# Optimization experiments

Measured on AMD Instinct MI355X. Metric: run time of the kernel, lower is better.

Reference implementation:

```python
import jax, jax.numpy as jnp
import numpy as np
import math

H_IMG, W_IMG = 800, 1216
STRIDES = [4, 8, 16, 32, 64]
SIZES = [32, 64, 128, 256, 512]
RATIOS = [0.5, 1.0, 2.0]
NUM_PER_LEVEL = [(-(-H_IMG // s)) * (-(-W_IMG // s)) * len(RATIOS) for s in STRIDES]
A_TOTAL = sum(NUM_PER_LEVEL)  # 728973
B = 4
PRE_NMS = 1000   # pre_nms_top_n['testing']
POST_NMS = 1000  # post_nms_top_n['testing']
NMS_TH = 0.7
MIN_SIZE = 1e-3
BBOX_XFORM_CLIP = math.log(1000.0 / 16)
NEG = -1e10
LEVELS_NP = np.repeat(np.arange(len(NUM_PER_LEVEL)), NUM_PER_LEVEL).astype(np.int32)


def _make_anchors():
    out = []
    for stride, size in zip(STRIDES, SIZES):
        fh, fw = -(-H_IMG // stride), -(-W_IMG // stride)
        r = np.sqrt(np.asarray(RATIOS, dtype=np.float64))
        ws, hs = size / r, size * r
        base = np.stack([-ws / 2, -hs / 2, ws / 2, hs / 2], axis=1)  # [3,4]
        sx = np.arange(fw, dtype=np.float64) * stride
        sy = np.arange(fh, dtype=np.float64) * stride
        gy, gx = np.meshgrid(sy, sx, indexing='ij')
        shifts = np.stack([gx.ravel(), gy.ravel(), gx.ravel(), gy.ravel()], axis=1)
        out.append((shifts[:, None, :] + base[None]).reshape(-1, 4))
    return np.concatenate(out, 0).astype(np.float32)


def setup_inputs() -> dict:
    key = jax.random.key(0)
    k1, k2 = jax.random.split(key)
    objectness = jax.random.normal(k1, (B, A_TOTAL), dtype=jnp.float32)
    deltas = jax.random.normal(k2, (B, A_TOTAL, 4), dtype=jnp.float32) * 0.2
    anchors = jnp.asarray(_make_anchors())
    return {'objectness': objectness, 'deltas': deltas, 'anchors': anchors}


def _decode(deltas, anchors):
    # BoxCoder.decode with weights (1,1,1,1)
    wa = anchors[:, 2] - anchors[:, 0]
    ha = anchors[:, 3] - anchors[:, 1]
    cxa = anchors[:, 0] + 0.5 * wa
    cya = anchors[:, 1] + 0.5 * ha
    dx, dy = deltas[..., 0], deltas[..., 1]
    dw = jnp.minimum(deltas[..., 2], BBOX_XFORM_CLIP)
    dh = jnp.minimum(deltas[..., 3], BBOX_XFORM_CLIP)
    cx = dx * wa + cxa
    cy = dy * ha + cya
    w = jnp.exp(dw) * wa
    h = jnp.exp(dh) * ha
    return jnp.stack([cx - 0.5 * w, cy - 0.5 * h, cx + 0.5 * w, cy + 0.5 * h], axis=-1)


def _topk_per_level(obj):
    # _get_top_n_idx: independent top-k within each anchor level, indices offset
    idxs, off = [], 0
    for n in NUM_PER_LEVEL:
        k = min(PRE_NMS, n)
        _, ti = jax.lax.top_k(obj[:, off:off + n], k)
        idxs.append(ti + off)
        off += n
    return jnp.concatenate(idxs, axis=1)


def _pairwise_iou(b):
    area = (b[:, 2] - b[:, 0]) * (b[:, 3] - b[:, 1])
    lt = jnp.maximum(b[:, None, :2], b[None, :, :2])
    rb = jnp.minimum(b[:, None, 2:], b[None, :, 2:])
    wh = jnp.clip(rb - lt, 0.0)
    inter = wh[..., 0] * wh[..., 1]
    return inter / (area[:, None] + area[None, :] - inter)


def _filter_image(boxes, scores, lvl):
    # clip_boxes_to_image
    x1 = jnp.clip(boxes[:, 0], 0.0, W_IMG)
    y1 = jnp.clip(boxes[:, 1], 0.0, H_IMG)
    x2 = jnp.clip(boxes[:, 2], 0.0, W_IMG)
    y2 = jnp.clip(boxes[:, 3], 0.0, H_IMG)
    boxes = jnp.stack([x1, y1, x2, y2], axis=1)
    # remove_small_boxes (as a validity mask; fixed shapes under jit)
    valid = ((x2 - x1) >= MIN_SIZE) & ((y2 - y1) >= MIN_SIZE)
    scores = jnp.where(valid, scores, NEG)
    N = boxes.shape[0]
    # batched_nms: offset boxes per level so levels never overlap
    sg_boxes = jax.lax.stop_gradient(boxes)
    offset = lvl.astype(boxes.dtype) * (sg_boxes.max() + 1.0)
    order = jnp.argsort(-jax.lax.stop_gradient(scores))
    iou = _pairwise_iou(sg_boxes[order] + offset[order][:, None])  # [N,N]
    idx = jnp.arange(N)
    def body(i, keep):
        sup = (iou[i] > NMS_TH) & keep[i] & (idx > i)
        return keep & ~sup
    keep = jax.lax.fori_loop(0, N, body, valid[order])
    # kept entries in score order, then truncate to POST_NMS (fixed shape)
    prio = jnp.where(keep, idx, N)
    sel = jnp.argsort(prio)[:POST_NMS]
    kept = keep[sel]
    src = order[sel]
    out_b = jnp.where(kept[:, None], boxes[src], 0.0)
    out_s = jnp.where(kept, scores[src], NEG)
    return out_b, out_s


def reference(objectness, deltas, anchors):
    proposals = _decode(deltas, anchors)                      # [B,A,4]
    top_idx = _topk_per_level(objectness)                     # [B,5000]
    obj_sel = jnp.take_along_axis(objectness, top_idx, axis=1)
    prop_sel = jnp.take_along_axis(proposals, top_idx[..., None], axis=1)
    lvl_sel = jnp.asarray(LEVELS_NP)[top_idx]
    boxes, scores = jax.vmap(_filter_image)(prop_sel, obj_sel, lvl_sel)
    return boxes, scores  # [B,POST_NMS,4], [B,POST_NMS]
```

## Files before the change

kernel.cpp:

```cpp
#include <hip/hip_runtime.h>
#include <stdint.h>

#pragma clang fp contract(off)

#define B_IMGS   4
#define NLVL     5
#define A_TOTAL  242991
#define NSEL     4741
#define NBUCK    8192
#define BSHIFT   19
#define CAND_CAP 2048
#define POST_NMS 1000
#define NBL      (B_IMGS * NLVL)
#define NMS_TH   0.7f
#define NEGV     (-1e10f)
#define W_IMGF   1216.0f
#define H_IMGF   800.0f
#define MIN_SZ   1e-3f
#define BBOX_CLIP 4.135166556742356f

__device__ __forceinline__ int lvl_k(int l) { return (l == 4) ? 741 : 1000; }

__device__ __forceinline__ unsigned flipf(float f) {
    unsigned u = __float_as_uint(f);
    return u ^ (unsigned)(((int)u >> 31) | 0x80000000);
}
__device__ __forceinline__ float unflipf(unsigned os) {
    unsigned u = (os & 0x80000000u) ? (os ^ 0x80000000u) : ~os;
    return __uint_as_float(u);
}

__device__ __forceinline__ void async_cp16(const void* g, void* l) {
    __builtin_amdgcn_global_load_lds(
        (const __attribute__((address_space(1))) unsigned*)g,
        (__attribute__((address_space(3))) unsigned*)l,
        16, 0, 0);
}

static constexpr size_t SZ_HIST    = (size_t)NBL * NBUCK * sizeof(unsigned);
static constexpr size_t OFF_CNT    = SZ_HIST;
static constexpr size_t OFF_BOXMAX = OFF_CNT + NBL * sizeof(unsigned);
static constexpr size_t ZERO_BYTES = OFF_BOXMAX + B_IMGS * sizeof(unsigned);
static constexpr size_t OFF_CAND   = (ZERO_BYTES + 15) & ~(size_t)15;
static constexpr size_t OFF_SEL    = OFF_CAND + (size_t)NBL * CAND_CAP * 8;
static constexpr size_t OFF_BOXR   = OFF_SEL + (size_t)B_IMGS * NSEL * 8;
static constexpr size_t OFF_SCR    = OFF_BOXR + (size_t)B_IMGS * NSEL * 16;
static constexpr size_t OFF_BOXL   = OFF_SCR + (size_t)B_IMGS * NSEL * 4;
static constexpr size_t OFF_VAL    = OFF_BOXL + (size_t)B_IMGS * NSEL * 16;
static constexpr size_t OFF_RMAP   = OFF_VAL + (size_t)B_IMGS * NSEL * 4;
static constexpr size_t OFF_KEEP   = OFF_RMAP + (size_t)B_IMGS * NSEL * 4;
static constexpr size_t OFF_MASK   = OFF_KEEP + (size_t)B_IMGS * NSEL * 4;
static constexpr size_t WS_NEED    = OFF_MASK + (size_t)NBL * 1024 * 16 * 8;

#define HBLK_PER_IMG 34
__global__ void k_hist(const float* __restrict__ obj, unsigned* __restrict__ hist) {
    __shared__ unsigned lh[NBUCK];
    const int tid = threadIdx.x;
    const int b = blockIdx.x / HBLK_PER_IMG;
    const int r = blockIdx.x - b * HBLK_PER_IMG;
    int l, sub, chunk, lstart, n;
    if (r < 24)      { l = 0; sub = r;      chunk = 7600; lstart = 0;      n = 182400; }
    else if (r < 30) { l = 1; sub = r - 24; chunk = 7600; lstart = 182400; n = 45600; }
    else if (r < 32) { l = 2; sub = r - 30; chunk = 5700; lstart = 228000; n = 11400; }
    else if (r == 32){ l = 3; sub = 0;      chunk = 2850; lstart = 239400; n = 2850; }
    else             { l = 4; sub = 0;      chunk = 741;  lstart = 242250; n = 741; }
    #pragma unroll
    for (int i = tid; i < NBUCK; i += 512) lh[i] = 0;
    __syncthreads();
    const int s0 = sub * chunk;
    const int cnt = min(chunk, n - s0);
    const float* src = obj + (size_t)b * A_TOTAL + lstart + s0;
    for (int i = tid; i < cnt; i += 512) {
        unsigned os = flipf(src[i]);
        atomicAdd(&lh[os >> BSHIFT], 1u);
    }
    __syncthreads();
    unsigned* gh = hist + (size_t)(b * NLVL + l) * NBUCK;
    for (int i = tid; i < NBUCK; i += 512) {
        unsigned v = lh[i];
        if (v) atomicAdd(&gh[i], v);
    }
}

#define CBLK_PER_IMG 65
__global__ void k_compact(const float* __restrict__ obj, const unsigned* __restrict__ hist,
                          unsigned* __restrict__ cnt, unsigned long long* __restrict__ cand) {
    __shared__ unsigned long long sbuf[CAND_CAP];
    __shared__ unsigned part[256];
    __shared__ unsigned chunkbuf[32];
    __shared__ int s_chunk;
    __shared__ unsigned s_cum, s_thr, lcnt, gbase;
    const int tid = threadIdx.x;
    const int b = blockIdx.x / CBLK_PER_IMG;
    const int r = blockIdx.x - b * CBLK_PER_IMG;
    int l, sub, chunk, lstart, n;
    if (r < 48)      { l = 0; sub = r;      chunk = 3800; lstart = 0;      n = 182400; }
    else if (r < 60) { l = 1; sub = r - 48; chunk = 3800; lstart = 182400; n = 45600; }
    else if (r < 63) { l = 2; sub = r - 60; chunk = 3800; lstart = 228000; n = 11400; }
    else if (r == 63){ l = 3; sub = 0;      chunk = 2850; lstart = 239400; n = 2850; }
    else             { l = 4; sub = 0;      chunk = 741;  lstart = 242250; n = 741; }
    const int bl = b * NLVL + l;
    const int kl = lvl_k(l);
    const unsigned* h = hist + (size_t)bl * NBUCK;
    {
        unsigned s = 0;
        for (int i = 0; i < 32; ++i) s += h[tid * 32 + i];
        part[tid] = s;
    }
    if (tid == 0) lcnt = 0;
    __syncthreads();
    if (tid == 0) {
        unsigned cum = 0;
        int t = 255;
        for (; t > 0; --t) {
            if (cum + part[t] >= (unsigned)kl) break;
            cum += part[t];
        }
        s_chunk = t;
        s_cum = cum;
    }
    __syncthreads();
    if (tid < 32) chunkbuf[tid] = h[s_chunk * 32 + tid];
    __syncthreads();
    if (tid == 0) {
        unsigned c2 = s_cum;
        int T = s_chunk * 32;
        for (int i = 31; i >= 0; --i) {
            c2 += chunkbuf[i];
            if (c2 >= (unsigned)kl) { T = s_chunk * 32 + i; break; }
        }
        s_thr = (unsigned)T;
    }
    __syncthreads();
    const unsigned T = s_thr;
    const int s0 = sub * chunk;
    const int m = min(chunk, n - s0);
    const int abase = lstart + s0;
    const float* src = obj + (size_t)b * A_TOTAL + abase;
    for (int i = tid; i < m; i += 256) {
        unsigned os = flipf(src[i]);
        if ((os >> BSHIFT) >= T) {
            unsigned slot = atomicAdd(&lcnt, 1u);
            if (slot < CAND_CAP)
                sbuf[slot] = (((unsigned long long)(~os)) << 32) | (unsigned)(abase + i);
        }
    }
    __syncthreads();
    unsigned total = lcnt; if (total > CAND_CAP) total = CAND_CAP;
    if (tid == 0) gbase = atomicAdd(&cnt[bl], total);
    __syncthreads();
    const unsigned gb = gbase;
    for (unsigned i = tid; i < total; i += 256) {
        unsigned g = gb + i;
        if (g < CAND_CAP)
            cand[(size_t)bl * CAND_CAP + g] = sbuf[i];
    }
}

__global__ void k_sortlevel(const unsigned long long* __restrict__ cand,
                            const unsigned* __restrict__ cnt,
                            unsigned long long* __restrict__ sel) {
    __shared__ unsigned long long keys[CAND_CAP];
    const int bl = blockIdx.x;
    const int b = bl / NLVL, l = bl - (bl / NLVL) * NLVL;
    const int tid = threadIdx.x;
    int m = (int)cnt[bl];
    if (m > CAND_CAP) m = CAND_CAP;
    for (int i = tid; i < CAND_CAP; i += 512)
        keys[i] = (i < m) ? cand[(size_t)bl * CAND_CAP + i] : ~0ULL;
    __syncthreads();
    for (int k = 2; k <= CAND_CAP; k <<= 1) {
        for (int j = k >> 1; j > 0; j >>= 1) {
            for (int t = tid; t < CAND_CAP / 2; t += 512) {
                int i = ((t / j) * (j << 1)) + (t % j);
                int p = i + j;
                bool up = ((i & k) == 0);
                unsigned long long a = keys[i], c = keys[p];
                if ((a > c) == up) { keys[i] = c; keys[p] = a; }
            }
            __syncthreads();
        }
    }
    int kl = lvl_k(l);
    for (int q = tid; q < kl; q += 512)
        sel[(size_t)b * NSEL + l * 1000 + q] = keys[q];
}

__device__ __forceinline__ int lbound_lds(const unsigned long long* s, int len,
                                          unsigned long long key) {
    int lo = 0, hi = len;
    while (lo < hi) {
        int mid = (lo + hi) >> 1;
        if (s[mid] < key) lo = mid + 1; else hi = mid;
    }
    return lo;
}

__global__ void k_decode(const float* __restrict__ deltas, const float* __restrict__ anchors,
                         const unsigned long long* __restrict__ sel,
                         float* __restrict__ boxes_r, float* __restrict__ score_r,
                         float* __restrict__ boxes_l, int* __restrict__ valid_l,
                         int* __restrict__ rankmap, unsigned* __restrict__ boxmax) {
    __shared__ unsigned long long skey[NSEL];
    __shared__ float wmax[16];
    const int b = blockIdx.y;
    const int tid = threadIdx.x;
    for (int i = tid; i < NSEL; i += 1024)
        skey[i] = sel[(size_t)b * NSEL + i];
    __syncthreads();

    int p = blockIdx.x * 1024 + tid;
    bool on = p < NSEL;
    float mx = 0.0f;
    if (on) {
        int l = p / 1000;
        int q = p - l * 1000;
        unsigned long long key = skey[p];
        unsigned a = (unsigned)(key & 0xFFFFFFFFu);
        unsigned os = ~((unsigned)(key >> 32));
        if (a >= A_TOTAL) a = 0;
        float score = unflipf(os);
        int r = q;
        for (int l2 = 0; l2 < NLVL; ++l2) {
            if (l2 == l) continue;
            r += lbound_lds(skey + l2 * 1000, lvl_k(l2), key);
        }
        const float* dv = deltas + ((size_t)b * A_TOTAL + a) * 4;
        const float* av = anchors + (size_t)a * 4;
        float ax1 = av[0], ay1 = av[1], ax2 = av[2], ay2 = av[3];
        float wa = ax2 - ax1, ha = ay2 - ay1;
        float cxa = ax1 + 0.5f * wa, cya = ay1 + 0.5f * ha;
        float dx = dv[0], dy = dv[1];
        float dw = fminf(dv[2], BBOX_CLIP), dh = fminf(dv[3], BBOX_CLIP);
        float cx = dx * wa + cxa, cy = dy * ha + cya;
        float w = expf(dw) * wa, h = expf(dh) * ha;
        float x1 = cx - 0.5f * w, y1 = cy - 0.5f * h;
        float x2 = cx + 0.5f * w, y2 = cy + 0.5f * h;
        float x1c = fminf(fmaxf(x1, 0.0f), W_IMGF);
        float y1c = fminf(fmaxf(y1, 0.0f), H_IMGF);
        float x2c = fminf(fmaxf(x2, 0.0f), W_IMGF);
        float y2c = fminf(fmaxf(y2, 0.0f), H_IMGF);
        int valid = ((x2c - x1c) >= MIN_SZ) && ((y2c - y1c) >= MIN_SZ);
        mx = fmaxf(fmaxf(x1c, y1c), fmaxf(x2c, y2c));
        size_t rp = (size_t)b * NSEL + r;
        boxes_r[rp * 4 + 0] = x1c; boxes_r[rp * 4 + 1] = y1c;
        boxes_r[rp * 4 + 2] = x2c; boxes_r[rp * 4 + 3] = y2c;
        score_r[rp] = score;
        size_t pp = (size_t)b * NSEL + p;
        boxes_l[pp * 4 + 0] = x1c; boxes_l[pp * 4 + 1] = y1c;
        boxes_l[pp * 4 + 2] = x2c; boxes_l[pp * 4 + 3] = y2c;
        valid_l[pp] = valid;
        rankmap[pp] = r;
    }
    #pragma unroll
    for (int o = 32; o > 0; o >>= 1)
        mx = fmaxf(mx, __shfl_xor(mx, o));
    if ((tid & 63) == 0) wmax[tid >> 6] = mx;
    __syncthreads();
    if (tid == 0) {
        float m2 = wmax[0];
        #pragma unroll
        for (int i = 1; i < 16; ++i) m2 = fmaxf(m2, wmax[i]);
        atomicMax(boxmax + b, __float_as_uint(m2));
    }
}

__global__ void k_mask(const float* __restrict__ boxes_l, const unsigned* __restrict__ boxmax,
                       unsigned long long* __restrict__ mask) {
    int bl = blockIdx.z;
    int b = bl / NLVL, l = bl - b * NLVL;
    int kl = lvl_k(l);
    int w = blockIdx.x, rg = blockIdx.y, tid = threadIdx.x;
    if (rg * 256 >= kl) return;
    float M = __uint_as_float(boxmax[b]) + 1.0f;
    float off = (float)l * M;
    __shared__ float cb[64][5];
    int j0 = w * 64;
    if (tid < 64) {
        int j = j0 + tid;
        if (j < kl) {
            const float* bp = boxes_l + ((size_t)b * NSEL + l * 1000 + j) * 4;
            float x1 = bp[0] + off, y1 = bp[1] + off, x2 = bp[2] + off, y2 = bp[3] + off;
            cb[tid][0] = x1; cb[tid][1] = y1; cb[tid][2] = x2; cb[tid][3] = y2;
            cb[tid][4] = (x2 - x1) * (y2 - y1);
        }
    }
    __syncthreads();
    int i = rg * 256 + tid;
    if (i >= kl) return;
    unsigned long long word = 0;
    if (j0 + 63 > i) {
        const float* bp = boxes_l + ((size_t)b * NSEL + l * 1000 + i) * 4;
        float ix1 = bp[0] + off, iy1 = bp[1] + off, ix2 = bp[2] + off, iy2 = bp[3] + off;
        float ai = (ix2 - ix1) * (iy2 - iy1);
        int jmax = min(64, kl - j0);
        for (int bb = 0; bb < jmax; ++bb) {
            int jj = j0 + bb;
            if (jj <= i) continue;
            float ltx = fmaxf(ix1, cb[bb][0]), lty = fmaxf(iy1, cb[bb][1]);
            float rbx = fminf(ix2, cb[bb][2]), rby = fminf(iy2, cb[bb][3]);
            float ww = fmaxf(rbx - ltx, 0.0f), hh = fmaxf(rby - lty, 0.0f);
            float inter = ww * hh;
            float iou = inter / ((ai + cb[bb][4]) - inter);
            if (iou > NMS_TH) word |= (1ULL << bb);
        }
    }
    mask[((size_t)bl * 1024 + i) * 16 + w] = word;
}

__global__ void k_resolve(const int* __restrict__ valid_l, const int* __restrict__ rankmap,
                          const unsigned long long* __restrict__ mask, int* __restrict__ keep_r) {
    const int bl = blockIdx.x;
    const int b = bl / NLVL, l = bl - b * NLVL;
    const int kl = lvl_k(l);
    const int lane = threadIdx.x;
    __shared__ __align__(16) unsigned long long sbufA[64 * 16];
    __shared__ __align__(16) unsigned long long sbufB[64 * 16];
    const int base = b * NSEL + l * 1000;

    unsigned long long keep_w = 0;
    for (int c = 0; c < 16; ++c) {
        int q = c * 64 + lane;
        int vv = (q < kl) ? valid_l[base + q] : 0;
        unsigned long long bm = __ballot(vv);
        if (lane == c) keep_w = bm;
    }

    const int nch = (kl + 63) >> 6;
    const char* mbyte = (const char*)(mask + (size_t)bl * 1024 * 16);

    {
        const char* g0 = mbyte + (size_t)lane * 16;
        #pragma unroll
        for (int j = 0; j < 8; ++j)
            async_cp16(g0 + j * 1024, (char*)sbufA + j * 1024);
    }

    for (int c = 0; c < nch; ++c) {
        unsigned long long* cur = (c & 1) ? sbufB : sbufA;
        unsigned long long* nxt = (c & 1) ? sbufA : sbufB;
        __syncthreads();
        if (c + 1 < nch) {
            const char* g1 = mbyte + (size_t)(c + 1) * 8192 + (size_t)lane * 16;
            #pragma unroll
            for (int j = 0; j < 8; ++j)
                async_cp16(g1 + j * 1024, (char*)nxt + j * 1024);
        }
        unsigned long long kw = __shfl(keep_w, c);
        if (kw) {
            unsigned long long diag = cur[lane * 16 + c];
            unsigned dlo = (unsigned)diag, dhi = (unsigned)(diag >> 32);
            unsigned long long nz = __ballot(diag != 0ULL);
            unsigned long long rem = kw & nz;
            while (rem) {
                int r = __ffsll((long long)rem) - 1;
                unsigned lo = __builtin_amdgcn_readlane(dlo, r);
                unsigned hi = __builtin_amdgcn_readlane(dhi, r);
                unsigned long long d = ((unsigned long long)hi << 32) | lo;
                kw &= ~d;
                rem &= ~(d | (1ULL << r));
            }
            unsigned long long supp = 0;
            if (lane < 16) {
                #pragma unroll
                for (int r = 0; r < 64; ++r) {
                    unsigned long long m = cur[r * 16 + lane];
                    supp |= (((kw >> r) & 1ULL) ? m : 0ULL);
                }
            }
            if (lane == c) keep_w = kw;
            else if (lane < 16 && lane > c) keep_w &= ~supp;
        }
    }
    __syncthreads();
    for (int c = 0; c < 16; ++c) {
        unsigned long long kwc = __shfl(keep_w, c);
        int q = c * 64 + lane;
        if (q < kl)
            keep_r[b * NSEL + rankmap[base + q]] = (int)((kwc >> lane) & 1ULL);
    }
}

__global__ void k_output(const int* __restrict__ keep_r, const float* __restrict__ boxes_r,
                         const float* __restrict__ score_r, float* __restrict__ out) {
    int b = blockIdx.x, tid = threadIdx.x;
    float* ob = out + (size_t)b * POST_NMS * 4;
    float* osc = out + (size_t)B_IMGS * POST_NMS * 4 + (size_t)b * POST_NMS;
    for (int p = tid; p < POST_NMS; p += 256) {
        ob[p * 4 + 0] = 0.0f; ob[p * 4 + 1] = 0.0f;
        ob[p * 4 + 2] = 0.0f; ob[p * 4 + 3] = 0.0f;
        osc[p] = NEGV;
    }
    __syncthreads();
    const int CH = 19;
    int base = tid * CH;
    int cnt = 0;
    for (int k = 0; k < CH; ++k) {
        int r = base + k;
        if (r < NSEL) cnt += keep_r[b * NSEL + r];
    }
    __shared__ int ps[256];
    ps[tid] = cnt;
    __syncthreads();
    for (int ofs = 1; ofs < 256; ofs <<= 1) {
        int v = (tid >= ofs) ? ps[tid - ofs] : 0;
        __syncthreads();
        ps[tid] += v;
        __syncthreads();
    }
    int p = ps[tid] - cnt;
    for (int k = 0; k < CH; ++k) {
        int r = base + k;
        if (r < NSEL && keep_r[b * NSEL + r]) {
            if (p < POST_NMS) {
                const float* bp = boxes_r + ((size_t)b * NSEL + r) * 4;
                ob[p * 4 + 0] = bp[0]; ob[p * 4 + 1] = bp[1];
                ob[p * 4 + 2] = bp[2]; ob[p * 4 + 3] = bp[3];
                osc[p] = score_r[(size_t)b * NSEL + r];
            }
            ++p;
        }
    }
}

extern "C" void kernel_launch(void* const* d_in, const int* in_sizes, int n_in,
                              void* d_out, int out_size, void* d_ws, size_t ws_size,
                              hipStream_t stream) {
    const float* obj     = (const float*)d_in[0];
    const float* deltas  = (const float*)d_in[1];
    const float* anchors = (const float*)d_in[2];
    float* out = (float*)d_out;

    char* ws = (char*)d_ws;
    unsigned*            hist    = (unsigned*)(ws);
    unsigned*            cnt     = (unsigned*)(ws + OFF_CNT);
    unsigned*            boxmax  = (unsigned*)(ws + OFF_BOXMAX);
    unsigned long long*  cand    = (unsigned long long*)(ws + OFF_CAND);
    unsigned long long*  sel     = (unsigned long long*)(ws + OFF_SEL);
    float*               boxes_r = (float*)(ws + OFF_BOXR);
    float*               score_r = (float*)(ws + OFF_SCR);
    float*               boxes_l = (float*)(ws + OFF_BOXL);
    int*                 valid_l = (int*)(ws + OFF_VAL);
    int*                 rankmap = (int*)(ws + OFF_RMAP);
    int*                 keep_r  = (int*)(ws + OFF_KEEP);
    unsigned long long*  maskp   = (unsigned long long*)(ws + OFF_MASK);

    (void)in_sizes; (void)n_in; (void)out_size; (void)ws_size; (void)WS_NEED;

    hipMemsetAsync(d_ws, 0, ZERO_BYTES, stream);

    k_hist<<<B_IMGS * HBLK_PER_IMG, 512, 0, stream>>>(obj, hist);
    k_compact<<<B_IMGS * CBLK_PER_IMG, 256, 0, stream>>>(obj, hist, cnt, cand);
    k_sortlevel<<<NBL, 512, 0, stream>>>(cand, cnt, sel);
    k_decode<<<dim3(5, B_IMGS), 1024, 0, stream>>>(
        deltas, anchors, sel, boxes_r, score_r, boxes_l, valid_l, rankmap, boxmax);
    k_mask<<<dim3(16, 4, NBL), 256, 0, stream>>>(boxes_l, boxmax, maskp);
    k_resolve<<<NBL, 64, 0, stream>>>(valid_l, rankmap, maskp, keep_r);
    k_output<<<B_IMGS, 256, 0, stream>>>(keep_r, boxes_r, score_r, out);
}
```

Baseline: 201.7 us.

## Fuse NMS mask build and resolve into one on-chip kernel per level

```diff
diff --git a/kernel.cpp b/kernel.cpp
--- a/kernel.cpp
+++ b/kernel.cpp
@@ -30,13 +30,6 @@
     return __uint_as_float(u);
 }
 
-__device__ __forceinline__ void async_cp16(const void* g, void* l) {
-    __builtin_amdgcn_global_load_lds(
-        (const __attribute__((address_space(1))) unsigned*)g,
-        (__attribute__((address_space(3))) unsigned*)l,
-        16, 0, 0);
-}
-
 static constexpr size_t SZ_HIST    = (size_t)NBL * NBUCK * sizeof(unsigned);
 static constexpr size_t OFF_CNT    = SZ_HIST;
 static constexpr size_t OFF_BOXMAX = OFF_CNT + NBL * sizeof(unsigned);
@@ -49,8 +42,7 @@
 static constexpr size_t OFF_VAL    = OFF_BOXL + (size_t)B_IMGS * NSEL * 16;
 static constexpr size_t OFF_RMAP   = OFF_VAL + (size_t)B_IMGS * NSEL * 4;
 static constexpr size_t OFF_KEEP   = OFF_RMAP + (size_t)B_IMGS * NSEL * 4;
-static constexpr size_t OFF_MASK   = OFF_KEEP + (size_t)B_IMGS * NSEL * 4;
-static constexpr size_t WS_NEED    = OFF_MASK + (size_t)NBL * 1024 * 16 * 8;
+static constexpr size_t WS_NEED    = OFF_KEEP + (size_t)B_IMGS * NSEL * 4;
 
 #define HBLK_PER_IMG 34
 __global__ void k_hist(const float* __restrict__ obj, unsigned* __restrict__ hist) {
@@ -166,23 +158,21 @@
     const int tid = threadIdx.x;
     int m = (int)cnt[bl];
     if (m > CAND_CAP) m = CAND_CAP;
-    for (int i = tid; i < CAND_CAP; i += 512)
+    for (int i = tid; i < CAND_CAP; i += 1024)
         keys[i] = (i < m) ? cand[(size_t)bl * CAND_CAP + i] : ~0ULL;
     __syncthreads();
     for (int k = 2; k <= CAND_CAP; k <<= 1) {
         for (int j = k >> 1; j > 0; j >>= 1) {
-            for (int t = tid; t < CAND_CAP / 2; t += 512) {
-                int i = ((t / j) * (j << 1)) + (t % j);
-                int p = i + j;
-                bool up = ((i & k) == 0);
-                unsigned long long a = keys[i], c = keys[p];
-                if ((a > c) == up) { keys[i] = c; keys[p] = a; }
-            }
+            int i = ((tid / j) * (j << 1)) + (tid % j);
+            int p = i + j;
+            bool up = ((i & k) == 0);
+            unsigned long long a = keys[i], c = keys[p];
+            if ((a > c) == up) { keys[i] = c; keys[p] = a; }
             __syncthreads();
         }
     }
     int kl = lvl_k(l);
-    for (int q = tid; q < kl; q += 512)
+    for (int q = tid; q < kl; q += 1024)
         sel[(size_t)b * NSEL + l * 1000 + q] = keys[q];
 }
 
@@ -265,92 +255,64 @@
     }
 }
 
-__global__ void k_mask(const float* __restrict__ boxes_l, const unsigned* __restrict__ boxmax,
-                       unsigned long long* __restrict__ mask) {
-    int bl = blockIdx.z;
-    int b = bl / NLVL, l = bl - b * NLVL;
-    int kl = lvl_k(l);
-    int w = blockIdx.x, rg = blockIdx.y, tid = threadIdx.x;
-    if (rg * 256 >= kl) return;
-    float M = __uint_as_float(boxmax[b]) + 1.0f;
-    float off = (float)l * M;
-    __shared__ float cb[64][5];
-    int j0 = w * 64;
-    if (tid < 64) {
-        int j = j0 + tid;
-        if (j < kl) {
-            const float* bp = boxes_l + ((size_t)b * NSEL + l * 1000 + j) * 4;
-            float x1 = bp[0] + off, y1 = bp[1] + off, x2 = bp[2] + off, y2 = bp[3] + off;
-            cb[tid][0] = x1; cb[tid][1] = y1; cb[tid][2] = x2; cb[tid][3] = y2;
-            cb[tid][4] = (x2 - x1) * (y2 - y1);
-        }
-    }
-    __syncthreads();
-    int i = rg * 256 + tid;
-    if (i >= kl) return;
-    unsigned long long word = 0;
-    if (j0 + 63 > i) {
-        const float* bp = boxes_l + ((size_t)b * NSEL + l * 1000 + i) * 4;
-        float ix1 = bp[0] + off, iy1 = bp[1] + off, ix2 = bp[2] + off, iy2 = bp[3] + off;
-        float ai = (ix2 - ix1) * (iy2 - iy1);
-        int jmax = min(64, kl - j0);
-        for (int bb = 0; bb < jmax; ++bb) {
-            int jj = j0 + bb;
-            if (jj <= i) continue;
-            float ltx = fmaxf(ix1, cb[bb][0]), lty = fmaxf(iy1, cb[bb][1]);
-            float rbx = fminf(ix2, cb[bb][2]), rby = fminf(iy2, cb[bb][3]);
-            float ww = fmaxf(rbx - ltx, 0.0f), hh = fmaxf(rby - lty, 0.0f);
-            float inter = ww * hh;
-            float iou = inter / ((ai + cb[bb][4]) - inter);
-            if (iou > NMS_TH) word |= (1ULL << bb);
-        }
-    }
-    mask[((size_t)bl * 1024 + i) * 16 + w] = word;
-}
-
-__global__ void k_resolve(const int* __restrict__ valid_l, const int* __restrict__ rankmap,
-                          const unsigned long long* __restrict__ mask, int* __restrict__ keep_r) {
+__global__ void k_nms(const float* __restrict__ boxes_l, const int* __restrict__ valid_l,
+                      const int* __restrict__ rankmap, const unsigned* __restrict__ boxmax,
+                      int* __restrict__ keep_r) {
+    __shared__ float sx1[1000], sy1[1000], sx2[1000], sy2[1000], sar[1000];
+    __shared__ unsigned long long keepw[16];
+    __shared__ unsigned long long diag[64];
     const int bl = blockIdx.x;
     const int b = bl / NLVL, l = bl - b * NLVL;
     const int kl = lvl_k(l);
-    const int lane = threadIdx.x;
-    __shared__ __align__(16) unsigned long long sbufA[64 * 16];
-    __shared__ __align__(16) unsigned long long sbufB[64 * 16];
+    const int t = threadIdx.x;
     const int base = b * NSEL + l * 1000;
-
-    unsigned long long keep_w = 0;
-    for (int c = 0; c < 16; ++c) {
-        int q = c * 64 + lane;
-        int vv = (q < kl) ? valid_l[base + q] : 0;
-        unsigned long long bm = __ballot(vv);
-        if (lane == c) keep_w = bm;
-    }
+    const float M = __uint_as_float(boxmax[b]) + 1.0f;
+    const float off = (float)l * M;
+
+    if (t < 16) keepw[t] = 0ULL;
+    __syncthreads();
+    if (t < kl) {
+        const float4 bx = *(const float4*)(boxes_l + (size_t)(base + t) * 4);
+        float x1 = bx.x + off, y1 = bx.y + off, x2 = bx.z + off, y2 = bx.w + off;
+        sx1[t] = x1; sy1[t] = y1; sx2[t] = x2; sy2[t] = y2;
+        sar[t] = (x2 - x1) * (y2 - y1);
+        if (valid_l[base + t])
+            atomicOr(&keepw[t >> 6], 1ULL << (t & 63));
+    }
+    __syncthreads();
 
     const int nch = (kl + 63) >> 6;
-    const char* mbyte = (const char*)(mask + (size_t)bl * 1024 * 16);
-
-    {
-        const char* g0 = mbyte + (size_t)lane * 16;
-        #pragma unroll
-        for (int j = 0; j < 8; ++j)
-            async_cp16(g0 + j * 1024, (char*)sbufA + j * 1024);
-    }
-
     for (int c = 0; c < nch; ++c) {
-        unsigned long long* cur = (c & 1) ? sbufB : sbufA;
-        unsigned long long* nxt = (c & 1) ? sbufA : sbufB;
-        __syncthreads();
-        if (c + 1 < nch) {
-            const char* g1 = mbyte + (size_t)(c + 1) * 8192 + (size_t)lane * 16;
-            #pragma unroll
-            for (int j = 0; j < 8; ++j)
-                async_cp16(g1 + j * 1024, (char*)nxt + j * 1024);
-        }
-        unsigned long long kw = __shfl(keep_w, c);
-        if (kw) {
-            unsigned long long diag = cur[lane * 16 + c];
-            unsigned dlo = (unsigned)diag, dhi = (unsigned)(diag >> 32);
-            unsigned long long nz = __ballot(diag != 0ULL);
+        if (t < 64) diag[t] = 0ULL;
+        __syncthreads();
+        {
+            int r = t >> 4, sg = t & 15;
+            int i = c * 64 + r;
+            if (i < kl) {
+                float ix1 = sx1[i], iy1 = sy1[i], ix2 = sx2[i], iy2 = sy2[i], ai = sar[i];
+                unsigned long long nib = 0;
+                #pragma unroll
+                for (int k = 0; k < 4; ++k) {
+                    int s = sg * 4 + k;
+                    int j = c * 64 + s;
+                    if (j > i && j < kl) {
+                        float ltx = fmaxf(ix1, sx1[j]), lty = fmaxf(iy1, sy1[j]);
+                        float rbx = fminf(ix2, sx2[j]), rby = fminf(iy2, sy2[j]);
+                        float ww = fmaxf(rbx - ltx, 0.0f), hh = fmaxf(rby - lty, 0.0f);
+                        float inter = ww * hh;
+                        float iou = inter / ((ai + sar[j]) - inter);
+                        if (iou > NMS_TH) nib |= (1ULL << s);
+                    }
+                }
+                if (nib) atomicOr(&diag[r], nib);
+            }
+        }
+        __syncthreads();
+        if (t < 64) {
+            unsigned long long dw = diag[t];
+            unsigned dlo = (unsigned)dw, dhi = (unsigned)(dw >> 32);
+            unsigned long long kw = keepw[c];
+            unsigned long long nz = __ballot(dw != 0ULL);
             unsigned long long rem = kw & nz;
             while (rem) {
                 int r = __ffsll((long long)rem) - 1;
@@ -360,24 +322,36 @@
                 kw &= ~d;
                 rem &= ~(d | (1ULL << r));
             }
-            unsigned long long supp = 0;
-            if (lane < 16) {
-                #pragma unroll
-                for (int r = 0; r < 64; ++r) {
-                    unsigned long long m = cur[r * 16 + lane];
-                    supp |= (((kw >> r) & 1ULL) ? m : 0ULL);
+            if (t == 0) keepw[c] = kw;
+        }
+        __syncthreads();
+        if (c + 1 < nch) {
+            unsigned long long kwc = keepw[c];
+            const int j = t;
+            const bool on = (j >= (c + 1) * 64) && (j < kl);
+            float jx1 = 0, jy1 = 0, jx2 = 0, jy2 = 0, aj = 0;
+            if (on) { jx1 = sx1[j]; jy1 = sy1[j]; jx2 = sx2[j]; jy2 = sy2[j]; aj = sar[j]; }
+            while (kwc) {
+                int r = __ffsll((long long)kwc) - 1;
+                kwc &= kwc - 1;
+                int i = c * 64 + r;
+                float ix1 = sx1[i], iy1 = sy1[i], ix2 = sx2[i], iy2 = sy2[i], ai = sar[i];
+                if (on) {
+                    float ltx = fmaxf(ix1, jx1), lty = fmaxf(iy1, jy1);
+                    float rbx = fminf(ix2, jx2), rby = fminf(iy2, jy2);
+                    float ww = fmaxf(rbx - ltx, 0.0f), hh = fmaxf(rby - lty, 0.0f);
+                    float inter = ww * hh;
+                    float iou = inter / ((ai + aj) - inter);
+                    if (iou > NMS_TH)
+                        atomicAnd(&keepw[j >> 6], ~(1ULL << (j & 63)));
                 }
             }
-            if (lane == c) keep_w = kw;
-            else if (lane < 16 && lane > c) keep_w &= ~supp;
-        }
-    }
-    __syncthreads();
-    for (int c = 0; c < 16; ++c) {
-        unsigned long long kwc = __shfl(keep_w, c);
-        int q = c * 64 + lane;
-        if (q < kl)
-            keep_r[b * NSEL + rankmap[base + q]] = (int)((kwc >> lane) & 1ULL);
+        }
+        __syncthreads();
+    }
+    if (t < kl) {
+        int bit = (int)((keepw[t >> 6] >> (t & 63)) & 1ULL);
+        keep_r[b * NSEL + rankmap[base + t]] = bit;
     }
 }
 
@@ -443,7 +417,6 @@
     int*                 valid_l = (int*)(ws + OFF_VAL);
     int*                 rankmap = (int*)(ws + OFF_RMAP);
     int*                 keep_r  = (int*)(ws + OFF_KEEP);
-    unsigned long long*  maskp   = (unsigned long long*)(ws + OFF_MASK);
 
     (void)in_sizes; (void)n_in; (void)out_size; (void)ws_size; (void)WS_NEED;
 
@@ -451,10 +424,9 @@
 
     k_hist<<<B_IMGS * HBLK_PER_IMG, 512, 0, stream>>>(obj, hist);
     k_compact<<<B_IMGS * CBLK_PER_IMG, 256, 0, stream>>>(obj, hist, cnt, cand);
-    k_sortlevel<<<NBL, 512, 0, stream>>>(cand, cnt, sel);
+    k_sortlevel<<<NBL, 1024, 0, stream>>>(cand, cnt, sel);
     k_decode<<<dim3(5, B_IMGS), 1024, 0, stream>>>(
         deltas, anchors, sel, boxes_r, score_r, boxes_l, valid_l, rankmap, boxmax);
-    k_mask<<<dim3(16, 4, NBL), 256, 0, stream>>>(boxes_l, boxmax, maskp);
-    k_resolve<<<NBL, 64, 0, stream>>>(valid_l, rankmap, maskp, keep_r);
+    k_nms<<<NBL, 1024, 0, stream>>>(boxes_l, valid_l, rankmap, boxmax, keep_r);
     k_output<<<B_IMGS, 256, 0, stream>>>(keep_r, boxes_r, score_r, out);
 }
```

Result: slower. 351.2 us (+74.1%).
